# Optimization experiments

Hardware: AMD Instinct MI355X
Metric: run time of the kernel (lower is better)

Reference implementation:

```python
import jax, jax.numpy as jnp
import numpy as np
import math

D_MODEL = 1024
NHEAD = 16
D_HEAD = D_MODEL // NHEAD
TAU = 300.0
DELTA = 5.0 * 60.0  # delta_minutes -> seconds


def setup_inputs() -> dict:
    key = jax.random.key(0)
    ks = jax.random.split(key, 10)
    B, M = 4, 2048
    H = jax.random.normal(ks[0], (B, M, D_MODEL), dtype=jnp.float32)
    patch_mask = jax.random.randint(ks[1], (B, M), 0, 2).astype(jnp.int32)
    s = 1.0 / math.sqrt(D_MODEL)
    Wq = jax.random.normal(ks[2], (D_MODEL, D_MODEL), dtype=jnp.float32) * s
    bq = jnp.zeros((D_MODEL,), dtype=jnp.float32)
    Wk = jax.random.normal(ks[3], (D_MODEL, D_MODEL), dtype=jnp.float32) * s
    bk = jnp.zeros((D_MODEL,), dtype=jnp.float32)
    Wv = jax.random.normal(ks[4], (D_MODEL, D_MODEL), dtype=jnp.float32) * s
    bv = jnp.zeros((D_MODEL,), dtype=jnp.float32)
    Wo = jax.random.normal(ks[5], (D_MODEL, D_MODEL), dtype=jnp.float32) * s
    bo = jnp.zeros((D_MODEL,), dtype=jnp.float32)
    return {"H": H, "patch_mask": patch_mask, "Wq": Wq, "bq": bq,
            "Wk": Wk, "bk": bk, "Wv": Wv, "bv": bv, "Wo": Wo, "bo": bo}


def _time_bias(M):
    idx = jnp.arange(M)
    dist = jnp.abs(idx[:, None] - idx[None, :]).astype(jnp.float32) * DELTA
    w = jnp.exp(-dist / max(TAU, 1e-6))
    return jnp.log(w + 1e-12)  # (M, M)


def reference(H, patch_mask, Wq, bq, Wk, bk, Wv, bv, Wo, bo):
    B, M, D = H.shape
    nh, dh = NHEAD, D_HEAD
    # projections -> (B, nh, M, dh)
    q = (H @ Wq.T + bq).reshape(B, M, nh, dh).transpose(0, 2, 1, 3)
    k = (H @ Wk.T + bk).reshape(B, M, nh, dh).transpose(0, 2, 1, 3)
    v = (H @ Wv.T + bv).reshape(B, M, nh, dh).transpose(0, 2, 1, 3)
    attn = jnp.einsum('bhqd,bhkd->bhqk', q, k) / math.sqrt(dh)
    attn = attn + _time_bias(M)[None, None, :, :]
    key_pad = patch_mask <= 0  # (B, M)
    attn = jnp.where(key_pad[:, None, None, :], -1e9, attn)
    A = jax.nn.softmax(attn, axis=-1)
    out = jnp.einsum('bhqk,bhkd->bhqd', A, v)
    out = out.transpose(0, 2, 1, 3).reshape(B, M, D)
    out = out @ Wo.T + bo
    out = out * patch_mask[:, :, None].astype(out.dtype)
    return out
```

## Files before the change

kernel.cpp:

```cpp
#include <hip/hip_runtime.h>
#include <stdint.h>

typedef short short8 __attribute__((ext_vector_type(8)));
typedef float f32x4 __attribute__((ext_vector_type(4)));

#define B_    4
#define M_    2048
#define D_    1024
#define NH_   16
#define DH_   64
#define LOG2E 1.44269504f

__device__ __forceinline__ short f2bf(float f) {
  union { float f; uint32_t u; } v; v.f = f;
  uint32_t r = (v.u + 0x7fffu + ((v.u >> 16) & 1u)) >> 16;
  return (short)r;
}

__device__ __forceinline__ void gl_lds16(const void* g, void* l) {
  __builtin_amdgcn_global_load_lds(
      (__attribute__((address_space(1))) void*)(g),
      (__attribute__((address_space(3))) void*)(l),
      16, 0, 0);
}

__device__ __forceinline__ f32x4 mfma16(short8 a, short8 b, f32x4 c) {
  return __builtin_amdgcn_mfma_f32_16x16x32_bf16(a, b, c, 0, 0, 0);
}

__global__ __launch_bounds__(256) void cvt_kernel(const float* __restrict__ src,
                                                  short* __restrict__ dst, int n4) {
  int i = blockIdx.x * 256 + threadIdx.x;
  if (i >= n4) return;
  float4 v = ((const float4*)src)[i];
  short4 o;
  o.x = f2bf(v.x); o.y = f2bf(v.y); o.z = f2bf(v.z); o.w = f2bf(v.w);
  ((short4*)dst)[i] = o;
}

__global__ __launch_bounds__(256) void cvt4_kernel(const float* __restrict__ s0,
                                                   const float* __restrict__ s1,
                                                   const float* __restrict__ s2,
                                                   const float* __restrict__ s3,
                                                   short* __restrict__ d0,
                                                   short* __restrict__ d1,
                                                   short* __restrict__ d2,
                                                   short* __restrict__ d3, int n4) {
  const int y = blockIdx.y;
  const float* src = (y == 0) ? s0 : (y == 1) ? s1 : (y == 2) ? s2 : s3;
  short* dst = (y == 0) ? d0 : (y == 1) ? d1 : (y == 2) ? d2 : d3;
  int i = blockIdx.x * 256 + threadIdx.x;
  if (i >= n4) return;
  float4 v = ((const float4*)src)[i];
  short4 o;
  o.x = f2bf(v.x); o.y = f2bf(v.y); o.z = f2bf(v.z); o.w = f2bf(v.w);
  ((short4*)dst)[i] = o;
}

__global__ __launch_bounds__(256) void gemm_qkv(const short* __restrict__ A,
                                                const short* __restrict__ Wqb,
                                                const short* __restrict__ Wkb,
                                                const short* __restrict__ Wvb,
                                                const float* __restrict__ bq,
                                                const float* __restrict__ bk,
                                                const float* __restrict__ bv,
                                                short* __restrict__ Qo,
                                                short* __restrict__ Ko,
                                                short* __restrict__ Vo) {
  __shared__ char smem_raw[34816];
  short* Abuf = (short*)smem_raw;
  short* Bbuf = (short*)smem_raw + 4096;

  const int L = blockIdx.x + 8 * (blockIdx.y + 64 * blockIdx.z);
  const int xcd = L & 7;
  const int s = L >> 3;
  const int m_local = s & 7;
  const int nz = s >> 3;
  const int nt = nz & 7, z = nz >> 3;
  const int m0 = (xcd * 8 + m_local) * 128;
  const int n0 = nt * 128;

  const short* Bt = (z == 0) ? Wqb : (z == 1) ? Wkb : Wvb;
  const float* bias = (z == 0) ? bq : (z == 1) ? bk : bv;
  const float scale = (z == 0) ? 0.125f : 1.0f;

  const int tid = threadIdx.x;
  const int w = tid >> 6, l = tid & 63;
  const int q4 = l >> 4, c = l & 15;
  const int wr = w >> 1, wc = w & 1;

  f32x4 acc[4][4] = {};
  const int arow = (l >> 2);
  const int acol = (l & 3) * 8;

  for (int kk = 0; kk < 32; ++kk) {
    const int k0 = kk * 32;
#pragma unroll
    for (int st = 0; st < 2; ++st) {
      const int chunk = w * 2 + st;
      gl_lds16(A + (size_t)(m0 + chunk * 16 + arow) * 1024 + k0 + acol,
               Abuf + chunk * 512);
      gl_lds16(Bt + (size_t)(n0 + chunk * 16 + arow) * 1024 + k0 + acol,
               Bbuf + chunk * 512);
    }
    __syncthreads();
    short8 af[4], bfr[4];
#pragma unroll
    for (int i = 0; i < 4; ++i)
      af[i] = *(const short8*)(Abuf + (wr * 64 + i * 16 + c) * 32 + q4 * 8);
#pragma unroll
    for (int j = 0; j < 4; ++j)
      bfr[j] = *(const short8*)(Bbuf + (wc * 64 + j * 16 + c) * 32 + q4 * 8);
#pragma unroll
    for (int i = 0; i < 4; ++i)
#pragma unroll
      for (int j = 0; j < 4; ++j)
        acc[i][j] = mfma16(af[i], bfr[j], acc[i][j]);
    __syncthreads();
  }

  if (z < 2) {
    short* Cb = (short*)smem_raw;
    short* out = (z == 0) ? Qo : Ko;
#pragma unroll
    for (int j = 0; j < 4; ++j) {
      const float bvv = bias[n0 + wc * 64 + j * 16 + c];
#pragma unroll
      for (int i = 0; i < 4; ++i)
#pragma unroll
        for (int r = 0; r < 4; ++r)
          Cb[(wr * 64 + i * 16 + q4 * 4 + r) * 136 + wc * 64 + j * 16 + c] =
              f2bf((acc[i][j][r] + bvv) * scale);
    }
    __syncthreads();
#pragma unroll
    for (int p = 0; p < 8; ++p) {
      const int g = p * 256 + tid;
      const int row = g >> 4, seg = g & 15;
      *(short8*)(out + (size_t)(m0 + row) * 1024 + n0 + seg * 8) =
          *(const short8*)(Cb + row * 136 + seg * 8);
    }
  } else {
    short* Cb = (short*)smem_raw;
#pragma unroll
    for (int j = 0; j < 4; ++j) {
      const float bvv = bias[n0 + wc * 64 + j * 16 + c];
#pragma unroll
      for (int i = 0; i < 4; ++i) {
        short4 pk;
        pk.x = f2bf(acc[i][j][0] + bvv);
        pk.y = f2bf(acc[i][j][1] + bvv);
        pk.z = f2bf(acc[i][j][2] + bvv);
        pk.w = f2bf(acc[i][j][3] + bvv);
        *(short4*)(Cb + (wc * 64 + j * 16 + c) * 136 + wr * 64 + i * 16 + q4 * 4) = pk;
      }
    }
    __syncthreads();
    const int bb = m0 >> 11;
    const int tokb = m0 & 2047;
#pragma unroll
    for (int p = 0; p < 8; ++p) {
      const int g = p * 256 + tid;
      const int col = g >> 4, rseg = g & 15;
      const int colg = n0 + col;
      const int hh = colg >> 6, dd = colg & 63;
      *(short8*)(Vo + ((size_t)(bb * NH_ + hh) * DH_ + dd) * M_ + tokb + rseg * 8) =
          *(const short8*)(Cb + col * 136 + rseg * 8);
    }
  }
}

__global__ __launch_bounds__(256) void gemm_oproj(const short* __restrict__ A,
                                                  const short* __restrict__ Bt,
                                                  const float* __restrict__ bias,
                                                  const int* __restrict__ pmask,
                                                  float* __restrict__ outp) {
  __shared__ char smem_raw[34816];
  short* Abuf = (short*)smem_raw;
  short* Bbuf = (short*)smem_raw + 4096;

  const int L = blockIdx.x + 8 * blockIdx.y;
  const int xcd = L & 7;
  const int s = L >> 3;
  const int m_local = s & 7;
  const int nt = s >> 3;
  const int m0 = (xcd * 8 + m_local) * 128;
  const int n0 = nt * 128;

  const int tid = threadIdx.x;
  const int w = tid >> 6, l = tid & 63;
  const int q4 = l >> 4, c = l & 15;
  const int wr = w >> 1, wc = w & 1;

  f32x4 acc[4][4] = {};
  const int arow = (l >> 2);
  const int acol = (l & 3) * 8;

  for (int kk = 0; kk < 32; ++kk) {
    const int k0 = kk * 32;
#pragma unroll
    for (int st = 0; st < 2; ++st) {
      const int chunk = w * 2 + st;
      gl_lds16(A + (size_t)(m0 + chunk * 16 + arow) * 1024 + k0 + acol,
               Abuf + chunk * 512);
      gl_lds16(Bt + (size_t)(n0 + chunk * 16 + arow) * 1024 + k0 + acol,
               Bbuf + chunk * 512);
    }
    __syncthreads();
    short8 af[4], bfr[4];
#pragma unroll
    for (int i = 0; i < 4; ++i)
      af[i] = *(const short8*)(Abuf + (wr * 64 + i * 16 + c) * 32 + q4 * 8);
#pragma unroll
    for (int j = 0; j < 4; ++j)
      bfr[j] = *(const short8*)(Bbuf + (wc * 64 + j * 16 + c) * 32 + q4 * 8);
#pragma unroll
    for (int i = 0; i < 4; ++i)
#pragma unroll
      for (int j = 0; j < 4; ++j)
        acc[i][j] = mfma16(af[i], bfr[j], acc[i][j]);
    __syncthreads();
  }

  float* Cf = (float*)smem_raw;
#pragma unroll
  for (int half = 0; half < 2; ++half) {
    __syncthreads();
    if (wr == half) {
#pragma unroll
      for (int j = 0; j < 4; ++j) {
        const float bvv = bias[n0 + wc * 64 + j * 16 + c];
#pragma unroll
        for (int i = 0; i < 4; ++i)
#pragma unroll
          for (int r = 0; r < 4; ++r)
            Cf[(i * 16 + q4 * 4 + r) * 132 + wc * 64 + j * 16 + c] =
                acc[i][j][r] + bvv;
      }
    }
    __syncthreads();
#pragma unroll
    for (int p = 0; p < 8; ++p) {
      const int g = p * 256 + tid;
      const int row = g >> 5, seg = g & 31;
      const int rowg = m0 + half * 64 + row;
      const float mmv = (pmask[rowg] > 0) ? 1.0f : 0.0f;
      float4 v = *(const float4*)(Cf + row * 132 + seg * 4);
      v.x *= mmv; v.y *= mmv; v.z *= mmv; v.w *= mmv;
      *(float4*)(outp + (size_t)rowg * 1024 + n0 + seg * 4) = v;
    }
  }
}

__global__ __launch_bounds__(256) void attn_kernel(const short* __restrict__ Qb,
                                                   const short* __restrict__ Kb,
                                                   const short* __restrict__ Vtb,
                                                   const int* __restrict__ pmask,
                                                   short* __restrict__ Attb) {
  __shared__ short Pbuf[4][16 * 32];
  const int tid = threadIdx.x;
  const int w = tid >> 6, l = tid & 63;
  const int q4 = l >> 4, c = l & 15;
  const int qt = blockIdx.x, h = blockIdx.y, b = blockIdx.z;
  const short* Qrow = Qb + (size_t)(b * M_) * D_ + h * DH_;
  const short* Krow = Kb + (size_t)(b * M_) * D_ + h * DH_;
  const short* Vbh = Vtb + (size_t)(b * NH_ + h) * DH_ * M_;
  const int qrow0 = qt * 64 + w * 16;

  short8 aq0 = *(const short8*)(Qrow + (size_t)(qrow0 + c) * D_ + q4 * 8);
  short8 aq1 = *(const short8*)(Qrow + (size_t)(qrow0 + c) * D_ + 32 + q4 * 8);

  f32x4 o[4] = {};
  float lrun[4] = {0.f, 0.f, 0.f, 0.f};

  const int jt0 = max(0, 2 * qt - 2);
  const int jt1 = min(M_ / 32 - 1, 2 * qt + 3);

  for (int jt = jt0; jt <= jt1; ++jt) {
    const int j0 = jt * 32;
    short8 b00 = *(const short8*)(Krow + (size_t)(j0 + c) * D_ + q4 * 8);
    short8 b10 = *(const short8*)(Krow + (size_t)(j0 + c) * D_ + 32 + q4 * 8);
    short8 b01 = *(const short8*)(Krow + (size_t)(j0 + 16 + c) * D_ + q4 * 8);
    short8 b11 = *(const short8*)(Krow + (size_t)(j0 + 16 + c) * D_ + 32 + q4 * 8);
    f32x4 s0 = {}, s1 = {};
    s0 = mfma16(aq0, b00, s0);
    s0 = mfma16(aq1, b10, s0);
    s1 = mfma16(aq0, b01, s1);
    s1 = mfma16(aq1, b11, s1);

    const float w0m = (pmask[b * M_ + j0 + c] > 0) ? 1.f : 0.f;
    const float w1m = (pmask[b * M_ + j0 + 16 + c] > 0) ? 1.f : 0.f;

#pragma unroll
    for (int r = 0; r < 4; ++r) {
      const int qr = qrow0 + q4 * 4 + r;
      const float d0 = fminf(fabsf((float)(qr - (j0 + c))), 28.0f);
      const float d1 = fminf(fabsf((float)(qr - (j0 + 16 + c))), 28.0f);
      const float p0 = exp2f((s0[r] - d0) * LOG2E) * w0m;
      const float p1 = exp2f((s1[r] - d1) * LOG2E) * w1m;
      Pbuf[w][(q4 * 4 + r) * 32 + c] = f2bf(p0);
      Pbuf[w][(q4 * 4 + r) * 32 + 16 + c] = f2bf(p1);
      lrun[r] += p0 + p1;
    }
    short8 pa = *(const short8*)(&Pbuf[w][c * 32 + q4 * 8]);
#pragma unroll
    for (int f = 0; f < 4; ++f) {
      short8 bv = *(const short8*)(Vbh + (size_t)(f * 16 + c) * M_ + j0 + q4 * 8);
      o[f] = mfma16(pa, bv, o[f]);
    }
  }

#pragma unroll
  for (int r = 0; r < 4; ++r) {
#pragma unroll
    for (int off = 1; off < 16; off <<= 1)
      lrun[r] += __shfl_xor(lrun[r], off);
  }

#pragma unroll
  for (int r = 0; r < 4; ++r) {
    const float inv = 1.0f / lrun[r];
    const int tok = qrow0 + q4 * 4 + r;
#pragma unroll
    for (int f = 0; f < 4; ++f) {
      Attb[((size_t)(b * M_ + tok)) * D_ + h * DH_ + f * 16 + c] =
          f2bf(o[f][r] * inv);
    }
  }
}

extern "C" void kernel_launch(void* const* d_in, const int* in_sizes, int n_in,
                              void* d_out, int out_size, void* d_ws, size_t ws_size,
                              hipStream_t stream) {
  const float* H     = (const float*)d_in[0];
  const int*   pmask = (const int*)d_in[1];
  const float* Wq    = (const float*)d_in[2];
  const float* bq    = (const float*)d_in[3];
  const float* Wk    = (const float*)d_in[4];
  const float* bk    = (const float*)d_in[5];
  const float* Wv    = (const float*)d_in[6];
  const float* bv    = (const float*)d_in[7];
  const float* Wo    = (const float*)d_in[8];
  const float* bo    = (const float*)d_in[9];
  float* out = (float*)d_out;
  char* ws = (char*)d_ws;

  short* Hb   = (short*)(ws);
  short* Attb = (short*)(ws);
  short* Wqb  = (short*)(ws + (16u << 20));
  short* Wkb  = (short*)(ws + (18u << 20));
  short* Wvb  = (short*)(ws + (20u << 20));
  short* Wob  = (short*)(ws + (22u << 20));
  short* Qb   = (short*)(ws + (24u << 20));
  short* Kb2  = (short*)(ws + (40u << 20));
  short* Vtb  = (short*)(ws + (56u << 20));

  const int nH4 = B_ * M_ * D_ / 4;
  const int nW4 = D_ * D_ / 4;
  cvt_kernel<<<nH4 / 256, 256, 0, stream>>>(H, Hb, nH4);
  cvt4_kernel<<<dim3(nW4 / 256, 4), 256, 0, stream>>>(Wq, Wk, Wv, Wo,
                                                      Wqb, Wkb, Wvb, Wob, nW4);

  dim3 gq(8, 64, 3);
  gemm_qkv<<<gq, 256, 0, stream>>>(Hb, Wqb, Wkb, Wvb, bq, bk, bv, Qb, Kb2, Vtb);

  attn_kernel<<<dim3(M_ / 64, NH_, B_), 256, 0, stream>>>(Qb, Kb2, Vtb, pmask, Attb);

  gemm_oproj<<<dim3(8, 64), 256, 0, stream>>>(Attb, Wob, bo, pmask, out);
}
```

Baseline: 258.0 us.

## Stage attention Q/K/V tiles through LDS, fuse conversion kernels, raise GEMM occupancy

```diff
diff --git a/kernel.cpp b/kernel.cpp
--- a/kernel.cpp
+++ b/kernel.cpp
@@ -28,45 +28,44 @@
   return __builtin_amdgcn_mfma_f32_16x16x32_bf16(a, b, c, 0, 0, 0);
 }
 
-__global__ __launch_bounds__(256) void cvt_kernel(const float* __restrict__ src,
-                                                  short* __restrict__ dst, int n4) {
-  int i = blockIdx.x * 256 + threadIdx.x;
-  if (i >= n4) return;
+__global__ __launch_bounds__(256) void cvt_all(const float* __restrict__ H,
+                                               const float* __restrict__ s0,
+                                               const float* __restrict__ s1,
+                                               const float* __restrict__ s2,
+                                               const float* __restrict__ s3,
+                                               short* __restrict__ dH,
+                                               short* __restrict__ d0,
+                                               short* __restrict__ d1,
+                                               short* __restrict__ d2,
+                                               short* __restrict__ d3) {
+  const int bidx = blockIdx.x;
+  const float* src;
+  short* dst;
+  int i;
+  if (bidx < 8192) {
+    src = H; dst = dH; i = bidx * 256 + threadIdx.x;
+  } else {
+    const int y = (bidx - 8192) >> 10;
+    src = (y == 0) ? s0 : (y == 1) ? s1 : (y == 2) ? s2 : s3;
+    dst = (y == 0) ? d0 : (y == 1) ? d1 : (y == 2) ? d2 : d3;
+    i = ((bidx - 8192) & 1023) * 256 + threadIdx.x;
+  }
   float4 v = ((const float4*)src)[i];
   short4 o;
   o.x = f2bf(v.x); o.y = f2bf(v.y); o.z = f2bf(v.z); o.w = f2bf(v.w);
   ((short4*)dst)[i] = o;
 }
 
-__global__ __launch_bounds__(256) void cvt4_kernel(const float* __restrict__ s0,
-                                                   const float* __restrict__ s1,
-                                                   const float* __restrict__ s2,
-                                                   const float* __restrict__ s3,
-                                                   short* __restrict__ d0,
-                                                   short* __restrict__ d1,
-                                                   short* __restrict__ d2,
-                                                   short* __restrict__ d3, int n4) {
-  const int y = blockIdx.y;
-  const float* src = (y == 0) ? s0 : (y == 1) ? s1 : (y == 2) ? s2 : s3;
-  short* dst = (y == 0) ? d0 : (y == 1) ? d1 : (y == 2) ? d2 : d3;
-  int i = blockIdx.x * 256 + threadIdx.x;
-  if (i >= n4) return;
-  float4 v = ((const float4*)src)[i];
-  short4 o;
-  o.x = f2bf(v.x); o.y = f2bf(v.y); o.z = f2bf(v.z); o.w = f2bf(v.w);
-  ((short4*)dst)[i] = o;
-}
-
-__global__ __launch_bounds__(256) void gemm_qkv(const short* __restrict__ A,
-                                                const short* __restrict__ Wqb,
-                                                const short* __restrict__ Wkb,
-                                                const short* __restrict__ Wvb,
-                                                const float* __restrict__ bq,
-                                                const float* __restrict__ bk,
-                                                const float* __restrict__ bv,
-                                                short* __restrict__ Qo,
-                                                short* __restrict__ Ko,
-                                                short* __restrict__ Vo) {
+__global__ __launch_bounds__(256, 3) void gemm_qkv(const short* __restrict__ A,
+                                                   const short* __restrict__ Wqb,
+                                                   const short* __restrict__ Wkb,
+                                                   const short* __restrict__ Wvb,
+                                                   const float* __restrict__ bq,
+                                                   const float* __restrict__ bk,
+                                                   const float* __restrict__ bv,
+                                                   short* __restrict__ Qo,
+                                                   short* __restrict__ Ko,
+                                                   short* __restrict__ Vo) {
   __shared__ char smem_raw[34816];
   short* Abuf = (short*)smem_raw;
   short* Bbuf = (short*)smem_raw + 4096;
@@ -170,11 +169,11 @@
   }
 }
 
-__global__ __launch_bounds__(256) void gemm_oproj(const short* __restrict__ A,
-                                                  const short* __restrict__ Bt,
-                                                  const float* __restrict__ bias,
-                                                  const int* __restrict__ pmask,
-                                                  float* __restrict__ outp) {
+__global__ __launch_bounds__(256, 3) void gemm_oproj(const short* __restrict__ A,
+                                                     const short* __restrict__ Bt,
+                                                     const float* __restrict__ bias,
+                                                     const int* __restrict__ pmask,
+                                                     float* __restrict__ outp) {
   __shared__ char smem_raw[34816];
   short* Abuf = (short*)smem_raw;
   short* Bbuf = (short*)smem_raw + 4096;
@@ -257,31 +256,52 @@
                                                    const short* __restrict__ Vtb,
                                                    const int* __restrict__ pmask,
                                                    short* __restrict__ Attb) {
-  __shared__ short Pbuf[4][16 * 32];
+  __shared__ char smem[20480];
+  short* Qs = (short*)smem;
+  short* Ks = (short*)(smem + 8192);
+  short* Vs = (short*)(smem + 12288);
+  short* Ps = (short*)(smem + 16384);
+
   const int tid = threadIdx.x;
   const int w = tid >> 6, l = tid & 63;
   const int q4 = l >> 4, c = l & 15;
   const int qt = blockIdx.x, h = blockIdx.y, b = blockIdx.z;
-  const short* Qrow = Qb + (size_t)(b * M_) * D_ + h * DH_;
-  const short* Krow = Kb + (size_t)(b * M_) * D_ + h * DH_;
-  const short* Vbh = Vtb + (size_t)(b * NH_ + h) * DH_ * M_;
+  const short* Qbase = Qb + (size_t)(b * M_ + qt * 64) * D_ + h * DH_;
+  const short* Kbase = Kb + (size_t)(b * M_) * D_ + h * DH_;
+  const short* Vbase = Vtb + (size_t)(b * NH_ + h) * DH_ * M_;
   const int qrow0 = qt * 64 + w * 16;
 
-  short8 aq0 = *(const short8*)(Qrow + (size_t)(qrow0 + c) * D_ + q4 * 8);
-  short8 aq1 = *(const short8*)(Qrow + (size_t)(qrow0 + c) * D_ + 32 + q4 * 8);
+  const int jt0 = max(0, 2 * qt - 2);
+  const int jt1 = min(M_ / 32 - 1, 2 * qt + 3);
+
+#pragma unroll
+  for (int p = 0; p < 2; ++p) {
+    const int u = p * 256 + tid;
+    const int kh = u >> 8, row = (u >> 2) & 63, ch = u & 3;
+    gl_lds16(Qbase + (size_t)row * D_ + kh * 32 + ch * 8, (char*)Qs + u * 16);
+  }
+  {
+    const int j0 = jt0 * 32;
+    const int kh = tid >> 7, krow = (tid >> 2) & 31, ch = tid & 3;
+    gl_lds16(Kbase + (size_t)(j0 + krow) * D_ + kh * 32 + ch * 8, (char*)Ks + tid * 16);
+    const int vrow = tid >> 2;
+    gl_lds16(Vbase + (size_t)vrow * M_ + j0 + ch * 8, (char*)Vs + tid * 16);
+  }
+  __syncthreads();
+
+  short8 aq0 = *(const short8*)(Qs + (w * 16 + c) * 32 + q4 * 8);
+  short8 aq1 = *(const short8*)(Qs + 2048 + (w * 16 + c) * 32 + q4 * 8);
 
   f32x4 o[4] = {};
   float lrun[4] = {0.f, 0.f, 0.f, 0.f};
-
-  const int jt0 = max(0, 2 * qt - 2);
-  const int jt1 = min(M_ / 32 - 1, 2 * qt + 3);
+  short* Pw = Ps + w * 512;
 
   for (int jt = jt0; jt <= jt1; ++jt) {
     const int j0 = jt * 32;
-    short8 b00 = *(const short8*)(Krow + (size_t)(j0 + c) * D_ + q4 * 8);
-    short8 b10 = *(const short8*)(Krow + (size_t)(j0 + c) * D_ + 32 + q4 * 8);
-    short8 b01 = *(const short8*)(Krow + (size_t)(j0 + 16 + c) * D_ + q4 * 8);
-    short8 b11 = *(const short8*)(Krow + (size_t)(j0 + 16 + c) * D_ + 32 + q4 * 8);
+    short8 b00 = *(const short8*)(Ks + c * 32 + q4 * 8);
+    short8 b10 = *(const short8*)(Ks + 1024 + c * 32 + q4 * 8);
+    short8 b01 = *(const short8*)(Ks + (16 + c) * 32 + q4 * 8);
+    short8 b11 = *(const short8*)(Ks + 1024 + (16 + c) * 32 + q4 * 8);
     f32x4 s0 = {}, s1 = {};
     s0 = mfma16(aq0, b00, s0);
     s0 = mfma16(aq1, b10, s0);
@@ -298,15 +318,26 @@
       const float d1 = fminf(fabsf((float)(qr - (j0 + 16 + c))), 28.0f);
       const float p0 = exp2f((s0[r] - d0) * LOG2E) * w0m;
       const float p1 = exp2f((s1[r] - d1) * LOG2E) * w1m;
-      Pbuf[w][(q4 * 4 + r) * 32 + c] = f2bf(p0);
-      Pbuf[w][(q4 * 4 + r) * 32 + 16 + c] = f2bf(p1);
+      Pw[(q4 * 4 + r) * 32 + c] = f2bf(p0);
+      Pw[(q4 * 4 + r) * 32 + 16 + c] = f2bf(p1);
       lrun[r] += p0 + p1;
     }
-    short8 pa = *(const short8*)(&Pbuf[w][c * 32 + q4 * 8]);
+    short8 pa = *(const short8*)(Pw + c * 32 + q4 * 8);
 #pragma unroll
     for (int f = 0; f < 4; ++f) {
-      short8 bv = *(const short8*)(Vbh + (size_t)(f * 16 + c) * M_ + j0 + q4 * 8);
+      short8 bv = *(const short8*)(Vs + (f * 16 + c) * 32 + q4 * 8);
       o[f] = mfma16(pa, bv, o[f]);
+    }
+
+    if (jt < jt1) {
+      __syncthreads();
+      const int j0n = j0 + 32;
+      const int kh = tid >> 7, krow = (tid >> 2) & 31, ch = tid & 3;
+      gl_lds16(Kbase + (size_t)(j0n + krow) * D_ + kh * 32 + ch * 8,
+               (char*)Ks + tid * 16);
+      const int vrow = tid >> 2;
+      gl_lds16(Vbase + (size_t)vrow * M_ + j0n + ch * 8, (char*)Vs + tid * 16);
+      __syncthreads();
     }
   }
 
@@ -317,15 +348,22 @@
       lrun[r] += __shfl_xor(lrun[r], off);
   }
 
+  __syncthreads();
+  short* Cb = (short*)(smem + 8192);
 #pragma unroll
   for (int r = 0; r < 4; ++r) {
     const float inv = 1.0f / lrun[r];
-    const int tok = qrow0 + q4 * 4 + r;
-#pragma unroll
-    for (int f = 0; f < 4; ++f) {
-      Attb[((size_t)(b * M_ + tok)) * D_ + h * DH_ + f * 16 + c] =
-          f2bf(o[f][r] * inv);
-    }
+#pragma unroll
+    for (int f = 0; f < 4; ++f)
+      Cb[(w * 16 + q4 * 4 + r) * 72 + f * 16 + c] = f2bf(o[f][r] * inv);
+  }
+  __syncthreads();
+#pragma unroll
+  for (int p = 0; p < 2; ++p) {
+    const int u = p * 256 + tid;
+    const int row = u >> 3, seg = u & 7;
+    *(short8*)(Attb + (size_t)(b * M_ + qt * 64 + row) * D_ + h * DH_ + seg * 8) =
+        *(const short8*)(Cb + row * 72 + seg * 8);
   }
 }
 
@@ -355,11 +393,8 @@
   short* Kb2  = (short*)(ws + (40u << 20));
   short* Vtb  = (short*)(ws + (56u << 20));
 
-  const int nH4 = B_ * M_ * D_ / 4;
-  const int nW4 = D_ * D_ / 4;
-  cvt_kernel<<<nH4 / 256, 256, 0, stream>>>(H, Hb, nH4);
-  cvt4_kernel<<<dim3(nW4 / 256, 4), 256, 0, stream>>>(Wq, Wk, Wv, Wo,
-                                                      Wqb, Wkb, Wvb, Wob, nW4);
+  cvt_all<<<8192 + 4096, 256, 0, stream>>>(H, Wq, Wk, Wv, Wo,
+                                           Hb, Wqb, Wkb, Wvb, Wob);
 
   dim3 gq(8, 64, 3);
   gemm_qkv<<<gq, 256, 0, stream>>>(Hb, Wqb, Wkb, Wvb, bq, bk, bv, Qb, Kb2, Vtb);
```

After: 222.4 us. -13.8%, faster.
